# Kernel optimization log

Hardware: AMD Instinct MI355X
Metric: run time of the kernel (lower is better)

The kernel has to match this reference:

```python
import jax, jax.numpy as jnp
import numpy as np
from jax import lax

T, B, DIM, H, OUT = 512, 128, 512, 1024, 512


def setup_inputs() -> dict:
    key = jax.random.key(0)
    ks = jax.random.split(key, 7)
    s = lambda fan_in: 1.0 / np.sqrt(fan_in)
    return {
        "x": jax.random.normal(ks[0], (T, B, DIM), dtype=jnp.float32),
        "h0": jnp.zeros((B, H), dtype=jnp.float32),
        "Wx_w": jax.random.uniform(ks[1], (H, DIM), jnp.float32, -s(DIM), s(DIM)),
        "Wx_b": jax.random.uniform(ks[2], (H,), jnp.float32, -s(DIM), s(DIM)),
        "Wh_w": jax.random.uniform(ks[3], (H, H), jnp.float32, -s(H), s(H)),
        "Wh_b": jax.random.uniform(ks[4], (H,), jnp.float32, -s(H), s(H)),
        "Wo_w": jax.random.uniform(ks[5], (OUT, H), jnp.float32, -s(H), s(H)),
        "Wo_b": jax.random.uniform(ks[6], (OUT,), jnp.float32, -s(H), s(H)),
    }


def reference(x, h0, Wx_w, Wx_b, Wh_w, Wh_b, Wo_w, Wo_b):
    # Precompute the input projection for all timesteps in one big GEMM:
    # [T,B,DIM] @ [DIM,H] -> [T,B,H]  (Wx(x_t) + bias, includes Wh bias fused)
    xproj = jnp.einsum("tbd,hd->tbh", x, Wx_w) + Wx_b + Wh_b

    def step(h, xp_t):
        # h_{t} = tanh(Wh h_{t-1} + Wx x_t + biases)
        h_new = jnp.tanh(h @ Wh_w.T + xp_t)
        return h_new, h_new

    h_last, hs = lax.scan(step, h0, xproj)  # hs: [T,B,H]
    all_h = jnp.concatenate([h0[None], hs], axis=0)  # [T+1,B,H]
    # decode: F(Wo h_t) with F = sigmoid, batched over all steps
    all_y = jax.nn.sigmoid(jnp.einsum("tbh,oh->tbo", hs, Wo_w) + Wo_b)
    last_logits = h_last @ Wo_w.T + Wo_b  # Wo(all_h[-1]) without F
    return all_h, all_y, last_logits
```

## Files before the change

### kernel.cpp

```cpp
#include <hip/hip_runtime.h>
#include <hip/hip_bf16.h>

static constexpr int T_ = 512, B_ = 128, DIM_ = 512, H_ = 1024, OUT_ = 512;
static constexpr size_t BH = (size_t)B_ * H_;
static constexpr size_t HH = (size_t)H_ * H_;
static constexpr unsigned int SENT = 0xFFFFFFFFu;

using short8 = __attribute__((ext_vector_type(8))) short;
using f32x4  = __attribute__((ext_vector_type(4))) float;

__device__ __forceinline__ unsigned short f32_to_bf16(float x) {
    unsigned int u = __float_as_uint(x);
    u += 0x7fffu + ((u >> 16) & 1u);
    return (unsigned short)(u >> 16);
}
__device__ __forceinline__ float bf16_to_f32(unsigned short h) {
    return __uint_as_float(((unsigned int)h) << 16);
}

__global__ void copy_h0_kernel(const float* __restrict__ h0, float* __restrict__ out) {
    int i = blockIdx.x * blockDim.x + threadIdx.x;
    if (i < B_ * H_) out[i] = h0[i];
}

__global__ void cvt_planes_kernel(const float* __restrict__ src,
                                  unsigned short* __restrict__ hi,
                                  unsigned short* __restrict__ lo, int n4)
{
    int i = blockIdx.x * blockDim.x + threadIdx.x;
    if (i >= n4) return;
    const float4 v = *(const float4*)(src + (size_t)i * 4);
    unsigned short h[4] = {f32_to_bf16(v.x), f32_to_bf16(v.y),
                           f32_to_bf16(v.z), f32_to_bf16(v.w)};
    unsigned short l[4] = {f32_to_bf16(v.x - bf16_to_f32(h[0])),
                           f32_to_bf16(v.y - bf16_to_f32(h[1])),
                           f32_to_bf16(v.z - bf16_to_f32(h[2])),
                           f32_to_bf16(v.w - bf16_to_f32(h[3]))};
    *(ushort4*)(hi + (size_t)i * 4) = make_ushort4(h[0], h[1], h[2], h[3]);
    *(ushort4*)(lo + (size_t)i * 4) = make_ushort4(l[0], l[1], l[2], l[3]);
}

__global__ void pack_plane_kernel(const float* __restrict__ src,
                                  unsigned int* __restrict__ q, int n)
{
    int i = blockIdx.x * blockDim.x + threadIdx.x;
    if (i >= n) return;
    const float v = src[i];
    const unsigned short hi = f32_to_bf16(v);
    const unsigned short lo = f32_to_bf16(v - bf16_to_f32(hi));
    q[i] = (unsigned int)hi | ((unsigned int)lo << 16);
}

template<int SPLIT, int NB, int ACT>
__launch_bounds__(256)
__global__ void mfma_gemm(const float* __restrict__ A, const float* __restrict__ W,
                          const float* __restrict__ b1, const float* __restrict__ b2,
                          float* __restrict__ outp, int M, int N, int K)
{
    __shared__ unsigned short Ahi[128 * 32], Alo[SPLIT ? 128 * 32 : 1];
    __shared__ unsigned short Bhi[128 * 32], Blo[SPLIT ? 128 * 32 : 1];

    const int tid  = threadIdx.x;
    const int col0 = blockIdx.x * 128;
    const int row0 = blockIdx.y * 128;

    const int wv   = tid >> 6;
    const int lane = tid & 63;
    const int wr   = (wv >> 1) * 64;
    const int wc   = (wv & 1) * 64;

    f32x4 acc[4][4];
    #pragma unroll
    for (int i = 0; i < 4; ++i)
        #pragma unroll
        for (int j = 0; j < 4; ++j) acc[i][j] = (f32x4){0.f, 0.f, 0.f, 0.f};

    auto frag_off = [](int row, int unit) -> int {
        return row * 32 + ((unit ^ ((row >> 1) & 3)) << 3);
    };

    for (int k0 = 0; k0 < K; k0 += 32) {
        __syncthreads();
        #pragma unroll
        for (int i = 0; i < 4; ++i) {
            const int fid = tid + i * 256;
            const int row = fid >> 3;
            const int f4  = fid & 7;
            const int unit = f4 >> 1;
            const int uoff = ((unit ^ ((row >> 1) & 3)) << 3) + (f4 & 1) * 4;

            float4 av = *(const float4*)(A + (size_t)(row0 + row) * K + k0 + f4 * 4);
            float4 wvv = *(const float4*)(W + (size_t)(col0 + row) * K + k0 + f4 * 4);

            unsigned short ah[4] = {f32_to_bf16(av.x), f32_to_bf16(av.y),
                                    f32_to_bf16(av.z), f32_to_bf16(av.w)};
            unsigned short bh[4] = {f32_to_bf16(wvv.x), f32_to_bf16(wvv.y),
                                    f32_to_bf16(wvv.z), f32_to_bf16(wvv.w)};
            *(ushort4*)&Ahi[row * 32 + uoff] = make_ushort4(ah[0], ah[1], ah[2], ah[3]);
            *(ushort4*)&Bhi[row * 32 + uoff] = make_ushort4(bh[0], bh[1], bh[2], bh[3]);

            if constexpr (SPLIT) {
                unsigned short al[4] = {
                    f32_to_bf16(av.x - bf16_to_f32(ah[0])),
                    f32_to_bf16(av.y - bf16_to_f32(ah[1])),
                    f32_to_bf16(av.z - bf16_to_f32(ah[2])),
                    f32_to_bf16(av.w - bf16_to_f32(ah[3]))};
                unsigned short bl[4] = {
                    f32_to_bf16(wvv.x - bf16_to_f32(bh[0])),
                    f32_to_bf16(wvv.y - bf16_to_f32(bh[1])),
                    f32_to_bf16(wvv.z - bf16_to_f32(bh[2])),
                    f32_to_bf16(wvv.w - bf16_to_f32(bh[3]))};
                *(ushort4*)&Alo[row * 32 + uoff] = make_ushort4(al[0], al[1], al[2], al[3]);
                *(ushort4*)&Blo[row * 32 + uoff] = make_ushort4(bl[0], bl[1], bl[2], bl[3]);
            }
        }
        __syncthreads();

        const int lrow = lane & 15;
        const int unit = lane >> 4;

        short8 bh_f[4], bl_f[4];
        #pragma unroll
        for (int fc = 0; fc < 4; ++fc) {
            bh_f[fc] = *(const short8*)&Bhi[frag_off(wc + fc * 16 + lrow, unit)];
            if constexpr (SPLIT)
                bl_f[fc] = *(const short8*)&Blo[frag_off(wc + fc * 16 + lrow, unit)];
        }
        #pragma unroll
        for (int fr = 0; fr < 4; ++fr) {
            const short8 ah_f = *(const short8*)&Ahi[frag_off(wr + fr * 16 + lrow, unit)];
            if constexpr (SPLIT) {
                const short8 al_f = *(const short8*)&Alo[frag_off(wr + fr * 16 + lrow, unit)];
                #pragma unroll
                for (int fc = 0; fc < 4; ++fc) {
                    acc[fr][fc] = __builtin_amdgcn_mfma_f32_16x16x32_bf16(ah_f, bh_f[fc], acc[fr][fc], 0, 0, 0);
                    acc[fr][fc] = __builtin_amdgcn_mfma_f32_16x16x32_bf16(ah_f, bl_f[fc], acc[fr][fc], 0, 0, 0);
                    acc[fr][fc] = __builtin_amdgcn_mfma_f32_16x16x32_bf16(al_f, bh_f[fc], acc[fr][fc], 0, 0, 0);
                }
            } else {
                #pragma unroll
                for (int fc = 0; fc < 4; ++fc)
                    acc[fr][fc] = __builtin_amdgcn_mfma_f32_16x16x32_bf16(ah_f, bh_f[fc], acc[fr][fc], 0, 0, 0);
            }
        }
    }

    const int ccol = lane & 15;
    const int crow = (lane >> 4) * 4;
    #pragma unroll
    for (int fr = 0; fr < 4; ++fr) {
        #pragma unroll
        for (int fc = 0; fc < 4; ++fc) {
            const int col = col0 + wc + fc * 16 + ccol;
            float bias = 0.f;
            if constexpr (NB >= 1) bias += b1[col];
            if constexpr (NB >= 2) bias += b2[col];
            #pragma unroll
            for (int j = 0; j < 4; ++j) {
                const int row = row0 + wr + fr * 16 + crow + j;
                float v = acc[fr][fc][j] + bias;
                if constexpr (ACT == 1) v = tanhf(v);
                else if constexpr (ACT == 2) v = 1.0f / (1.0f + expf(-v));
                outp[(size_t)row * N + col] = v;
            }
        }
    }
}

__global__ __launch_bounds__(512, 1)
void rnn_persistent(unsigned int* __restrict__ Ppk,
                    const unsigned short* __restrict__ Whi,
                    const unsigned short* __restrict__ Wlo,
                    float* __restrict__ all_h)
{
    __shared__ float red[8][16][33];

    const int tid  = threadIdx.x;
    const int bid  = blockIdx.x;
    const int y    = bid >> 5;
    const int x    = bid & 31;
    const int r0   = y * 16;
    const int c0   = x * 32;

    const int w    = tid >> 6;
    const int lane = tid & 63;
    const int lr   = lane & 15;
    const int kg   = lane >> 4;

    const int ep_r = tid >> 5, ep_c = tid & 31;
    const size_t ep_idx = (size_t)(r0 + ep_r) * H_ + (c0 + ep_c);

    const int kbase = w * 128 + kg * 8;
    short8 wb0h[4], wb0l[4], wb1h[4], wb1l[4];
    #pragma unroll
    for (int it = 0; it < 4; ++it) {
        const int ko = it * 32;
        wb0h[it] = *(const short8*)(Whi + (size_t)(c0 + lr) * H_ + kbase + ko);
        wb0l[it] = *(const short8*)(Wlo + (size_t)(c0 + lr) * H_ + kbase + ko);
        wb1h[it] = *(const short8*)(Whi + (size_t)(c0 + 16 + lr) * H_ + kbase + ko);
        wb1l[it] = *(const short8*)(Wlo + (size_t)(c0 + 16 + lr) * H_ + kbase + ko);
    }

    const size_t arow = (size_t)(r0 + lr) * H_ + kbase;

    for (int t = 0; t < T_; ++t) {
        float* __restrict__ hdst = all_h + (size_t)(t + 1) * BH;
        const float xpv = hdst[ep_idx];

        const unsigned int* abase = Ppk + (size_t)(t % 3) * BH + arow;
        uint4 c0v, c1v, c2v, c3v, c4v, c5v, c6v, c7v;
        int spins = 0;
        bool ok;
        do {
            asm volatile(
                "global_load_dwordx4 %0, %8, off sc0 sc1\n\t"
                "global_load_dwordx4 %1, %8, off offset:16 sc0 sc1\n\t"
                "global_load_dwordx4 %2, %8, off offset:128 sc0 sc1\n\t"
                "global_load_dwordx4 %3, %8, off offset:144 sc0 sc1\n\t"
                "global_load_dwordx4 %4, %8, off offset:256 sc0 sc1\n\t"
                "global_load_dwordx4 %5, %8, off offset:272 sc0 sc1\n\t"
                "global_load_dwordx4 %6, %8, off offset:384 sc0 sc1\n\t"
                "global_load_dwordx4 %7, %8, off offset:400 sc0 sc1\n\t"
                "s_waitcnt vmcnt(0)"
                : "=&v"(c0v), "=&v"(c1v), "=&v"(c2v), "=&v"(c3v),
                  "=&v"(c4v), "=&v"(c5v), "=&v"(c6v), "=&v"(c7v)
                : "v"(abase));
            ok = true;
            #define CHK(u) ok &= ((u).x != SENT) & ((u).y != SENT) & \
                                 ((u).z != SENT) & ((u).w != SENT)
            CHK(c0v); CHK(c1v); CHK(c2v); CHK(c3v);
            CHK(c4v); CHK(c5v); CHK(c6v); CHK(c7v);
            #undef CHK
            if (__all(ok)) break;
            if (++spins > (1 << 17)) break;
            __builtin_amdgcn_s_sleep(1);
        } while (true);

        {
            unsigned int* cp = Ppk + (size_t)((t + 2) % 3) * BH + ep_idx;
            const unsigned int sv = SENT;
            asm volatile("global_store_dword %0, %1, off sc0 sc1"
                         :: "v"(cp), "v"(sv));
        }

        f32x4 acc0 = {0.f, 0.f, 0.f, 0.f}, acc1 = {0.f, 0.f, 0.f, 0.f};
        const uint4 chunks[8] = {c0v, c1v, c2v, c3v, c4v, c5v, c6v, c7v};

        #pragma unroll
        for (int it = 0; it < 4; ++it) {
            short8 ah, al;
            #pragma unroll
            for (int j = 0; j < 4; ++j) {
                const unsigned int u0 = ((const unsigned int*)&chunks[2 * it])[j];
                const unsigned int u1 = ((const unsigned int*)&chunks[2 * it + 1])[j];
                ah[j]     = (short)(u0 & 0xffffu);
                al[j]     = (short)(u0 >> 16);
                ah[4 + j] = (short)(u1 & 0xffffu);
                al[4 + j] = (short)(u1 >> 16);
            }
            acc0 = __builtin_amdgcn_mfma_f32_16x16x32_bf16(ah, wb0h[it], acc0, 0, 0, 0);
            acc0 = __builtin_amdgcn_mfma_f32_16x16x32_bf16(ah, wb0l[it], acc0, 0, 0, 0);
            acc0 = __builtin_amdgcn_mfma_f32_16x16x32_bf16(al, wb0h[it], acc0, 0, 0, 0);
            acc0 = __builtin_amdgcn_mfma_f32_16x16x32_bf16(al, wb0l[it], acc0, 0, 0, 0);
            acc1 = __builtin_amdgcn_mfma_f32_16x16x32_bf16(ah, wb1h[it], acc1, 0, 0, 0);
            acc1 = __builtin_amdgcn_mfma_f32_16x16x32_bf16(ah, wb1l[it], acc1, 0, 0, 0);
            acc1 = __builtin_amdgcn_mfma_f32_16x16x32_bf16(al, wb1h[it], acc1, 0, 0, 0);
            acc1 = __builtin_amdgcn_mfma_f32_16x16x32_bf16(al, wb1l[it], acc1, 0, 0, 0);
        }

        #pragma unroll
        for (int j = 0; j < 4; ++j) {
            red[w][kg * 4 + j][lr]      = acc0[j];
            red[w][kg * 4 + j][16 + lr] = acc1[j];
        }
        __syncthreads();

        {
            float s = ((red[0][ep_r][ep_c] + red[1][ep_r][ep_c])
                     + (red[2][ep_r][ep_c] + red[3][ep_r][ep_c]))
                    + ((red[4][ep_r][ep_c] + red[5][ep_r][ep_c])
                     + (red[6][ep_r][ep_c] + red[7][ep_r][ep_c]));
            const float v = tanhf(s + xpv);
            hdst[ep_idx] = v;
            const unsigned short hi = f32_to_bf16(v);
            const unsigned short lo = f32_to_bf16(v - bf16_to_f32(hi));
            const unsigned int pk = (unsigned int)hi | ((unsigned int)lo << 16);
            unsigned int* qp = Ppk + (size_t)((t + 1) % 3) * BH + ep_idx;
            asm volatile("s_waitcnt vmcnt(0)\n\t"
                         "global_store_dword %0, %1, off sc0 sc1"
                         :: "v"(qp), "v"(pk));
        }
        __syncthreads();
    }
}

__global__ __launch_bounds__(512)
void step_v4(const unsigned short* __restrict__ Phi, const unsigned short* __restrict__ Plo,
             const unsigned short* __restrict__ Whi, const unsigned short* __restrict__ Wlo,
             float* __restrict__ hdst,
             unsigned short* __restrict__ Qhi, unsigned short* __restrict__ Qlo)
{
    __shared__ float red[8][16][33];

    const int tid  = threadIdx.x;
    const int c0   = blockIdx.x * 32;
    const int r0   = blockIdx.y * 16;
    const int w    = tid >> 6;
    const int lane = tid & 63;
    const int lr   = lane & 15;
    const int kg   = lane >> 4;

    const int ep_r = tid >> 5, ep_c = tid & 31;
    const size_t ep_idx = (size_t)(r0 + ep_r) * H_ + (c0 + ep_c);
    const float xpv = hdst[ep_idx];

    const int kbase = w * 128 + kg * 8;
    const unsigned short* pah = Phi + (size_t)(r0 + lr) * H_ + kbase;
    const unsigned short* pal = Plo + (size_t)(r0 + lr) * H_ + kbase;
    const unsigned short* pb0h = Whi + (size_t)(c0 + lr) * H_ + kbase;
    const unsigned short* pb0l = Wlo + (size_t)(c0 + lr) * H_ + kbase;
    const unsigned short* pb1h = Whi + (size_t)(c0 + 16 + lr) * H_ + kbase;
    const unsigned short* pb1l = Wlo + (size_t)(c0 + 16 + lr) * H_ + kbase;

    f32x4 acc0 = {0.f, 0.f, 0.f, 0.f}, acc1 = {0.f, 0.f, 0.f, 0.f};

    #pragma unroll
    for (int it = 0; it < 4; ++it) {
        const int ko = it * 32;
        const short8 ah  = *(const short8*)(pah + ko);
        const short8 al  = *(const short8*)(pal + ko);
        const short8 b0h = *(const short8*)(pb0h + ko);
        const short8 b0l = *(const short8*)(pb0l + ko);
        const short8 b1h = *(const short8*)(pb1h + ko);
        const short8 b1l = *(const short8*)(pb1l + ko);

        acc0 = __builtin_amdgcn_mfma_f32_16x16x32_bf16(ah, b0h, acc0, 0, 0, 0);
        acc0 = __builtin_amdgcn_mfma_f32_16x16x32_bf16(ah, b0l, acc0, 0, 0, 0);
        acc0 = __builtin_amdgcn_mfma_f32_16x16x32_bf16(al, b0h, acc0, 0, 0, 0);
        acc0 = __builtin_amdgcn_mfma_f32_16x16x32_bf16(al, b0l, acc0, 0, 0, 0);
        acc1 = __builtin_amdgcn_mfma_f32_16x16x32_bf16(ah, b1h, acc1, 0, 0, 0);
        acc1 = __builtin_amdgcn_mfma_f32_16x16x32_bf16(ah, b1l, acc1, 0, 0, 0);
        acc1 = __builtin_amdgcn_mfma_f32_16x16x32_bf16(al, b1h, acc1, 0, 0, 0);
        acc1 = __builtin_amdgcn_mfma_f32_16x16x32_bf16(al, b1l, acc1, 0, 0, 0);
    }

    #pragma unroll
    for (int j = 0; j < 4; ++j) {
        red[w][kg * 4 + j][lr]      = acc0[j];
        red[w][kg * 4 + j][16 + lr] = acc1[j];
    }
    __syncthreads();

    float s = ((red[0][ep_r][ep_c] + red[1][ep_r][ep_c])
             + (red[2][ep_r][ep_c] + red[3][ep_r][ep_c]))
            + ((red[4][ep_r][ep_c] + red[5][ep_r][ep_c])
             + (red[6][ep_r][ep_c] + red[7][ep_r][ep_c]));
    const float v = tanhf(s + xpv);
    hdst[ep_idx] = v;
    const unsigned short hi = f32_to_bf16(v);
    Qhi[ep_idx] = hi;
    Qlo[ep_idx] = f32_to_bf16(v - bf16_to_f32(hi));
}

extern "C" void kernel_launch(void* const* d_in, const int* in_sizes, int n_in,
                              void* d_out, int out_size, void* d_ws, size_t ws_size,
                              hipStream_t stream)
{
    const float* x    = (const float*)d_in[0];
    const float* h0   = (const float*)d_in[1];
    const float* Wx_w = (const float*)d_in[2];
    const float* Wx_b = (const float*)d_in[3];
    const float* Wh_w = (const float*)d_in[4];
    const float* Wh_b = (const float*)d_in[5];
    const float* Wo_w = (const float*)d_in[6];
    const float* Wo_b = (const float*)d_in[7];

    float* out   = (float*)d_out;
    float* all_h = out;
    float* all_y = out + (size_t)(T_ + 1) * BH;
    float* last  = all_y + (size_t)T_ * B_ * OUT_;

    copy_h0_kernel<<<dim3((B_*H_ + 255)/256), dim3(256), 0, stream>>>(h0, all_h);

    mfma_gemm<1, 2, 0><<<dim3(H_/128, (T_*B_)/128), dim3(256), 0, stream>>>(
        x, Wx_w, Wx_b, Wh_b, all_h + BH, T_*B_, H_, DIM_);

    const size_t need_pers = 2 * HH * sizeof(unsigned short)
                           + 3 * BH * sizeof(unsigned int);
    const size_t need_v4   = (2 * HH + 4 * BH) * sizeof(unsigned short);

    if (ws_size >= need_pers) {
        unsigned short* Whi = (unsigned short*)d_ws;
        unsigned short* Wlo = Whi + HH;
        unsigned int*   Ppk = (unsigned int*)(Whi + 2 * HH);

        cvt_planes_kernel<<<dim3((int)(HH/4/256)), dim3(256), 0, stream>>>(
            Wh_w, Whi, Wlo, (int)(HH/4));
        pack_plane_kernel<<<dim3((int)(BH/256)), dim3(256), 0, stream>>>(
            h0, Ppk, (int)BH);
        hipMemsetAsync(Ppk + BH, 0xFF, 2 * BH * sizeof(unsigned int), stream);

        rnn_persistent<<<dim3(256), dim3(512), 0, stream>>>(
            Ppk, Whi, Wlo, all_h);
    } else if (ws_size >= need_v4) {
        unsigned short* wsu = (unsigned short*)d_ws;
        unsigned short* Whi = wsu;
        unsigned short* Wlo = wsu + HH;
        unsigned short* P0h = wsu + 2 * HH;
        unsigned short* P0l = P0h + BH;
        unsigned short* P1h = P0l + BH;
        unsigned short* P1l = P1h + BH;

        cvt_planes_kernel<<<dim3((int)(HH/4/256)), dim3(256), 0, stream>>>(
            Wh_w, Whi, Wlo, (int)(HH/4));
        cvt_planes_kernel<<<dim3((int)(BH/4/256)), dim3(256), 0, stream>>>(
            h0, P0h, P0l, (int)(BH/4));

        for (int t = 0; t < T_; ++t) {
            unsigned short* ph = (t & 1) ? P1h : P0h;
            unsigned short* pl = (t & 1) ? P1l : P0l;
            unsigned short* qh = (t & 1) ? P0h : P1h;
            unsigned short* ql = (t & 1) ? P0l : P1l;
            step_v4<<<dim3(32, 8), dim3(512), 0, stream>>>(
                ph, pl, Whi, Wlo, all_h + (size_t)(t + 1) * BH, qh, ql);
        }
    }

    mfma_gemm<0, 1, 2><<<dim3(OUT_/128, (T_*B_)/128), dim3(256), 0, stream>>>(
        all_h + BH, Wo_w, Wo_b, nullptr, all_y, T_*B_, OUT_, H_);

    mfma_gemm<0, 1, 0><<<dim3(OUT_/128, 1), dim3(256), 0, stream>>>(
        all_h + (size_t)T_ * BH, Wo_w, Wo_b, nullptr, last, B_, OUT_, H_);
}
```

Baseline: 2.792 ms.

## Use four-slot state ring and double-buffered reduction to drop per-step barrier

```diff
diff --git a/kernel.cpp b/kernel.cpp
--- a/kernel.cpp
+++ b/kernel.cpp
@@ -173,7 +173,7 @@
                     const unsigned short* __restrict__ Wlo,
                     float* __restrict__ all_h)
 {
-    __shared__ float red[8][16][33];
+    __shared__ float red[2][8][16][33];
 
     const int tid  = threadIdx.x;
     const int bid  = blockIdx.x;
@@ -207,11 +207,10 @@
         float* __restrict__ hdst = all_h + (size_t)(t + 1) * BH;
         const float xpv = hdst[ep_idx];
 
-        const unsigned int* abase = Ppk + (size_t)(t % 3) * BH + arow;
+        const unsigned int* abase = Ppk + (size_t)(t & 3) * BH + arow;
         uint4 c0v, c1v, c2v, c3v, c4v, c5v, c6v, c7v;
         int spins = 0;
-        bool ok;
-        do {
+        while (true) {
             asm volatile(
                 "global_load_dwordx4 %0, %8, off sc0 sc1\n\t"
                 "global_load_dwordx4 %1, %8, off offset:16 sc0 sc1\n\t"
@@ -225,19 +224,18 @@
                 : "=&v"(c0v), "=&v"(c1v), "=&v"(c2v), "=&v"(c3v),
                   "=&v"(c4v), "=&v"(c5v), "=&v"(c6v), "=&v"(c7v)
                 : "v"(abase));
-            ok = true;
-            #define CHK(u) ok &= ((u).x != SENT) & ((u).y != SENT) & \
-                                 ((u).z != SENT) & ((u).w != SENT)
-            CHK(c0v); CHK(c1v); CHK(c2v); CHK(c3v);
-            CHK(c4v); CHK(c5v); CHK(c6v); CHK(c7v);
-            #undef CHK
-            if (__all(ok)) break;
+            unsigned int mx = 0u;
+            #define MX(u) mx = max(mx, max(max((u).x, (u).y), max((u).z, (u).w)))
+            MX(c0v); MX(c1v); MX(c2v); MX(c3v);
+            MX(c4v); MX(c5v); MX(c6v); MX(c7v);
+            #undef MX
+            if (__all(mx != SENT)) break;
             if (++spins > (1 << 17)) break;
             __builtin_amdgcn_s_sleep(1);
-        } while (true);
+        }
 
         {
-            unsigned int* cp = Ppk + (size_t)((t + 2) % 3) * BH + ep_idx;
+            unsigned int* cp = Ppk + (size_t)((t + 3) & 3) * BH + ep_idx;
             const unsigned int sv = SENT;
             asm volatile("global_store_dword %0, %1, off sc0 sc1"
                          :: "v"(cp), "v"(sv));
@@ -270,27 +268,25 @@
 
         #pragma unroll
         for (int j = 0; j < 4; ++j) {
-            red[w][kg * 4 + j][lr]      = acc0[j];
-            red[w][kg * 4 + j][16 + lr] = acc1[j];
+            red[t & 1][w][kg * 4 + j][lr]      = acc0[j];
+            red[t & 1][w][kg * 4 + j][16 + lr] = acc1[j];
         }
         __syncthreads();
 
         {
-            float s = ((red[0][ep_r][ep_c] + red[1][ep_r][ep_c])
-                     + (red[2][ep_r][ep_c] + red[3][ep_r][ep_c]))
-                    + ((red[4][ep_r][ep_c] + red[5][ep_r][ep_c])
-                     + (red[6][ep_r][ep_c] + red[7][ep_r][ep_c]));
+            float s = ((red[t & 1][0][ep_r][ep_c] + red[t & 1][1][ep_r][ep_c])
+                     + (red[t & 1][2][ep_r][ep_c] + red[t & 1][3][ep_r][ep_c]))
+                    + ((red[t & 1][4][ep_r][ep_c] + red[t & 1][5][ep_r][ep_c])
+                     + (red[t & 1][6][ep_r][ep_c] + red[t & 1][7][ep_r][ep_c]));
             const float v = tanhf(s + xpv);
-            hdst[ep_idx] = v;
             const unsigned short hi = f32_to_bf16(v);
             const unsigned short lo = f32_to_bf16(v - bf16_to_f32(hi));
             const unsigned int pk = (unsigned int)hi | ((unsigned int)lo << 16);
-            unsigned int* qp = Ppk + (size_t)((t + 1) % 3) * BH + ep_idx;
-            asm volatile("s_waitcnt vmcnt(0)\n\t"
-                         "global_store_dword %0, %1, off sc0 sc1"
+            unsigned int* qp = Ppk + (size_t)((t + 1) & 3) * BH + ep_idx;
+            asm volatile("global_store_dword %0, %1, off sc0 sc1"
                          :: "v"(qp), "v"(pk));
-        }
-        __syncthreads();
+            hdst[ep_idx] = v;
+        }
     }
 }
 
@@ -386,7 +382,7 @@
         x, Wx_w, Wx_b, Wh_b, all_h + BH, T_*B_, H_, DIM_);
 
     const size_t need_pers = 2 * HH * sizeof(unsigned short)
-                           + 3 * BH * sizeof(unsigned int);
+                           + 4 * BH * sizeof(unsigned int);
     const size_t need_v4   = (2 * HH + 4 * BH) * sizeof(unsigned short);
 
     if (ws_size >= need_pers) {
@@ -398,7 +394,7 @@
             Wh_w, Whi, Wlo, (int)(HH/4));
         pack_plane_kernel<<<dim3((int)(BH/256)), dim3(256), 0, stream>>>(
             h0, Ppk, (int)BH);
-        hipMemsetAsync(Ppk + BH, 0xFF, 2 * BH * sizeof(unsigned int), stream);
+        hipMemsetAsync(Ppk + BH, 0xFF, 3 * BH * sizeof(unsigned int), stream);
 
         rnn_persistent<<<dim3(256), dim3(512), 0, stream>>>(
             Ppk, Whi, Wlo, all_h);
```

Result: slower. 3.565 ms (+27.7%).
